# Kernel optimization log

Measured on AMD Instinct MI355X. Metric: run time of the kernel, lower is better.

## Reference

```python
import jax, jax.numpy as jnp
import numpy as np

N = 100000
E = 1600000
IN_C, HID, HEADS, OUT_C = 128, 64, 4, 2
NEG_SLOPE = 0.2


def setup_inputs() -> dict:
    key = jax.random.key(0)
    ks = jax.random.split(key, 10)
    def glorot(k, shape):
        fan = shape[0] + shape[-1]
        return jax.random.uniform(k, shape, jnp.float32, -1.0, 1.0) * np.sqrt(6.0 / fan)
    x = jax.random.normal(ks[0], (N, IN_C), jnp.float32)
    edge_index = jax.random.randint(ks[1], (2, E), 0, N, jnp.int64)
    return {
        "x": x,
        "edge_index": edge_index,
        "W1": glorot(ks[2], (IN_C, HID)),
        "b1": jnp.zeros((HID,), jnp.float32),
        "W2": glorot(ks[3], (HID, HEADS * HID)),
        "att_src": glorot(ks[4], (HEADS, HID)) ,
        "att_dst": glorot(ks[5], (HEADS, HID)),
        "b2": jnp.zeros((HEADS * HID,), jnp.float32),
        "W3": glorot(ks[6], (HEADS * HID, OUT_C)),
        "b3": jnp.zeros((OUT_C,), jnp.float32),
    }


def _add_self_loops(edge_index, n):
    loop = jnp.arange(n, dtype=edge_index.dtype)
    src = jnp.concatenate([edge_index[0], loop])
    dst = jnp.concatenate([edge_index[1], loop])
    return src, dst


def gcn_conv(x, W, b, src, dst, n):
    # x' = X W, then symmetric deg-normalized scatter-add (self-loops included)
    xw = x @ W
    deg = jax.ops.segment_sum(jnp.ones_like(dst, dtype=xw.dtype), dst, num_segments=n)
    dinv = jnp.where(deg > 0, jax.lax.rsqrt(deg), 0.0)
    norm = dinv[src] * dinv[dst]                      # [E2]
    out = jax.ops.segment_sum(xw[src] * norm[:, None], dst, num_segments=n)
    return out + b


def gat_conv(x, W, att_src, att_dst, b, src, dst, n, heads, ch):
    xw = (x @ W).reshape(n, heads, ch)                # [N, H, C]
    a_s = (xw * att_src).sum(-1)                      # [N, H]
    a_d = (xw * att_dst).sum(-1)
    e = jax.nn.leaky_relu(a_s[src] + a_d[dst], NEG_SLOPE)   # [E2, H]
    # segment softmax over incoming edges per destination node
    m = jax.ops.segment_max(e, dst, num_segments=n)
    m = jnp.where(jnp.isfinite(m), m, 0.0)
    e = jnp.exp(e - m[dst])
    den = jax.ops.segment_sum(e, dst, num_segments=n)
    alpha = e / (den[dst] + 1e-16)                    # [E2, H]
    out = jax.ops.segment_sum(xw[src] * alpha[:, :, None], dst, num_segments=n)
    return out.reshape(n, heads * ch) + b


def reference(x, edge_index, W1, b1, W2, att_src, att_dst, b2, W3, b3):
    n = x.shape[0]
    src, dst = _add_self_loops(edge_index, n)
    h = jax.nn.relu(gcn_conv(x, W1, b1, src, dst, n))
    h = jax.nn.elu(gat_conv(h, W2, att_src, att_dst, b2, src, dst, n, HEADS, HID))
    return gcn_conv(h, W3, b3, src, dst, n)
```

## Files before the change

### kernel.cpp

```cpp
#include <hip/hip_runtime.h>
#include <math.h>

#define N_NODES 100000
#define N_EDGES 1600000
#define E2      (N_NODES + N_EDGES)
#define IN_C    128
#define HID     64
#define HEADS   4
#define HH      256
#define OUT_C   2
#define NEG_SLOPE 0.2f

#define SB   1024
#define NSB  ((N_NODES + SB - 1) / SB)
#define NRANGE 8
#define RDIV   12500
#define BINS   RDIV
#define NBK    100
#define CHUNK  (N_EDGES / NBK)
#define CITER  ((CHUNK + 255) / 256)
#define NHB    (NRANGE * NBK)
#define RT     10
#define NT1    6250
#define NGEMM1 ((NT1 + 3) / 4)

typedef __attribute__((ext_vector_type(8))) short bf16x8;
typedef __attribute__((ext_vector_type(4))) float f32x4;

__device__ __forceinline__ float bf2f(unsigned short u) {
    return __uint_as_float(((unsigned)u) << 16);
}
__device__ __forceinline__ unsigned short f2bf(float f) {
    unsigned u = __float_as_uint(f);
    u += 0x7fffu + ((u >> 16) & 1u);
    return (unsigned short)(u >> 16);
}


__global__ __launch_bounds__(256) void k_prep(const float* __restrict__ W2,
        const float* __restrict__ W1,
        const float* __restrict__ att_src, const float* __restrict__ att_dst,
        unsigned short* __restrict__ W2t, unsigned short* __restrict__ wsdt,
        unsigned short* __restrict__ W1t) {
    int b = blockIdx.x, t = threadIdx.x;
    if (b < 64) {
        int g = b * 256 + t;
        int k = g >> 8, n = g & 255;
        W2t[n * 64 + k] = f2bf(W2[g]);
        return;
    }
    if (b < 66) {
        int g = (b - 64) * 256 + t;
        wsdt[512 + g] = 0;
        int k = g >> 3, o = g & 7;
        int h = o & 3;
        const float* att = (o < 4) ? att_src : att_dst;
        float acc = 0.f;
        const float* wrow = W2 + (size_t)k * HH + h * 64;
        const float* arow = att + h * 64;
        for (int c = 0; c < 64; ++c) acc = fmaf(wrow[c], arow[c], acc);
        wsdt[o * 64 + k] = f2bf(acc);
        return;
    }
    int g = (b - 66) * 256 + t;
    int k = g >> 6, n = g & 63;
    W1t[n * 128 + k] = f2bf(W1[g]);
}

__global__ __launch_bounds__(256) void k_hista(const int* __restrict__ ei,
        unsigned short* __restrict__ hp16,
        const float* __restrict__ x, const unsigned short* __restrict__ W1t,
        unsigned short* __restrict__ xw1b) {
    __shared__ unsigned int hh[BINS];
    int b = blockIdx.x, t = threadIdx.x;
    if (b < NHB) {
        int r = b / NBK, k = b - r * NBK;
        for (int i = t; i < BINS; i += 256) hh[i] = 0u;
        __syncthreads();
        const int* dp = ei + N_EDGES + (size_t)k * CHUNK;
        int lo = r * RDIV;
        for (int it = 0; it < CITER; ++it) {
            int idx = it * 256 + t;
            if (idx < CHUNK) {
                int d = dp[idx] - lo;
                if ((unsigned)d < (unsigned)RDIV) atomicAdd(&hh[d], 1u);
            }
        }
        __syncthreads();
        unsigned short* hp = hp16 + (size_t)b * BINS;
        for (int i = t; i < BINS; i += 256) hp[i] = (unsigned short)hh[i];
        return;
    }
    int lane = t & 63, wv = t >> 6;
    int m = lane & 15, quad = lane >> 4;
    bf16x8 B[4][4];
#pragma unroll
    for (int ct = 0; ct < 4; ++ct)
#pragma unroll
        for (int ks = 0; ks < 4; ++ks)
            B[ct][ks] = *(const bf16x8*)(W1t + (size_t)(ct * 16 + m) * IN_C
                                         + ks * 32 + quad * 8);
    int tile = (b - NHB) * 4 + wv;
    if (tile >= NT1) return;
    int rbase = tile * 16;
    const float* xp = x + (size_t)(rbase + m) * IN_C + quad * 8;
    f32x4 c0 = {0.f, 0.f, 0.f, 0.f}, c1 = c0, c2 = c0, c3 = c0;
#pragma unroll
    for (int ks = 0; ks < 4; ++ks) {
        float4 f0 = *(const float4*)(xp + ks * 32);
        float4 f1 = *(const float4*)(xp + ks * 32 + 4);
        bf16x8 a;
        a[0] = (short)f2bf(f0.x); a[1] = (short)f2bf(f0.y);
        a[2] = (short)f2bf(f0.z); a[3] = (short)f2bf(f0.w);
        a[4] = (short)f2bf(f1.x); a[5] = (short)f2bf(f1.y);
        a[6] = (short)f2bf(f1.z); a[7] = (short)f2bf(f1.w);
        c0 = __builtin_amdgcn_mfma_f32_16x16x32_bf16(a, B[0][ks], c0, 0, 0, 0);
        c1 = __builtin_amdgcn_mfma_f32_16x16x32_bf16(a, B[1][ks], c1, 0, 0, 0);
        c2 = __builtin_amdgcn_mfma_f32_16x16x32_bf16(a, B[2][ks], c2, 0, 0, 0);
        c3 = __builtin_amdgcn_mfma_f32_16x16x32_bf16(a, B[3][ks], c3, 0, 0, 0);
    }
    int row0 = rbase + quad * 4;
#pragma unroll
    for (int ct = 0; ct < 4; ++ct) {
        f32x4 c = (ct == 0) ? c0 : (ct == 1) ? c1 : (ct == 2) ? c2 : c3;
        unsigned short* p = xw1b + (size_t)row0 * HID + ct * 16 + m;
#pragma unroll
        for (int r = 0; r < 4; ++r) p[(size_t)r * HID] = f2bf(c[r]);
    }
}

__global__ __launch_bounds__(256) void k_scan1(unsigned short* __restrict__ hp16,
        int* __restrict__ cnt, int* __restrict__ bsum) {
    int b = blockIdx.x, t = threadIdx.x;
    int s = 0;
#pragma unroll
    for (int u = 0; u < 4; ++u) {
        int i = b * SB + u * 256 + t;
        if (i < N_NODES) {
            int r = i / RDIV, bin = i - r * RDIV;
            unsigned short* p = hp16 + (size_t)r * NBK * BINS + bin;
            unsigned acc = 0;
            for (int k = 0; k < NBK; ++k) {
                unsigned short hv = p[(size_t)k * BINS];
                p[(size_t)k * BINS] = (unsigned short)acc;
                acc += hv;
            }
            cnt[i] = (int)acc;
            s += (int)acc + 1;
        }
    }
#pragma unroll
    for (int off = 1; off < 64; off <<= 1) s += __shfl_xor(s, off);
    __shared__ int wsum[4];
    int lane = t & 63, wv = t >> 6;
    if (lane == 0) wsum[wv] = s;
    __syncthreads();
    if (t == 0) bsum[b] = (wsum[0] + wsum[1]) + (wsum[2] + wsum[3]);
}

__global__ __launch_bounds__(256) void k_scan3(const int* __restrict__ cnt,
        const int* __restrict__ bsum, int* __restrict__ rowptr,
        float* __restrict__ dinv, int* __restrict__ col) {
    int b = blockIdx.x, t = threadIdx.x;
    int lane = t & 63, wv = t >> 6;
    __shared__ int wred[4];
    {
        int v = (t < b) ? bsum[t] : 0;
#pragma unroll
        for (int off = 1; off < 64; off <<= 1) v += __shfl_xor(v, off);
        if (lane == 0) wred[wv] = v;
    }
    __syncthreads();
    int pre = (wred[0] + wred[1]) + (wred[2] + wred[3]);
    __syncthreads();

    int i = b * SB + t * 4;
    int c0 = 0, c1 = 0, c2 = 0, c3 = 0;
    if (i + 3 < N_NODES) {
        int4 v = *(const int4*)(cnt + i);
        c0 = v.x; c1 = v.y; c2 = v.z; c3 = v.w;
    } else if (i < N_NODES) {
        c0 = cnt[i];
        if (i + 1 < N_NODES) c1 = cnt[i + 1];
        if (i + 2 < N_NODES) c2 = cnt[i + 2];
    }
    int n0 = (i < N_NODES), n1 = (i + 1 < N_NODES),
        n2 = (i + 2 < N_NODES), n3 = (i + 3 < N_NODES);
    int d0 = c0 + n0, d1 = c1 + n1, d2 = c2 + n2, d3 = c3 + n3;
    int s = (d0 + d1) + (d2 + d3);
    int inc = s;
#pragma unroll
    for (int off = 1; off < 64; off <<= 1) {
        int u = __shfl_up(inc, off);
        if (lane >= off) inc += u;
    }
    __shared__ int wtot[4];
    if (lane == 63) wtot[wv] = inc;
    __syncthreads();
    int base = pre + (inc - s);
    for (int w = 0; w < wv; ++w) base += wtot[w];
    if (n0) { rowptr[i]     = base;                dinv[i]     = rsqrtf((float)d0); col[base] = i; }
    if (n1) { rowptr[i + 1] = base + d0;           dinv[i + 1] = rsqrtf((float)d1); col[base + d0] = i + 1; }
    if (n2) { rowptr[i + 2] = base + d0 + d1;      dinv[i + 2] = rsqrtf((float)d2); col[base + d0 + d1] = i + 2; }
    if (n3) { rowptr[i + 3] = base + d0 + d1 + d2; dinv[i + 3] = rsqrtf((float)d3); col[base + d0 + d1 + d2] = i + 3; }
    if (b == 0 && t == 0) rowptr[N_NODES] = E2;
}

__global__ __launch_bounds__(256) void k_fillb(const int* __restrict__ ei,
        const int* __restrict__ rowptr, const unsigned short* __restrict__ hp16,
        int* __restrict__ col) {
    __shared__ unsigned int cur[BINS];
    int b = blockIdx.x, t = threadIdx.x;
    int r = b / NBK, k = b - r * NBK;
    int lo = r * RDIV;
    const unsigned short* pp = hp16 + (size_t)b * BINS;
    for (int i = t; i < BINS; i += 256)
        cur[i] = (unsigned)rowptr[lo + i] + 1u + (unsigned)pp[i];
    __syncthreads();
    const int* dp = ei + N_EDGES + (size_t)k * CHUNK;
    const int* sp = ei + (size_t)k * CHUNK;
    for (int it = 0; it < CITER; ++it) {
        int idx = it * 256 + t;
        if (idx < CHUNK) {
            int d = dp[idx] - lo;
            if ((unsigned)d < (unsigned)RDIV) {
                unsigned pos = atomicAdd(&cur[d], 1u);
                col[pos] = sp[idx];
            }
        }
    }
}

__global__ __launch_bounds__(256) void k_agg1(const int* __restrict__ rowptr,
        const int* __restrict__ col, const unsigned short* __restrict__ xw1b,
        const float* __restrict__ dinv, const float* __restrict__ b1,
        unsigned short* __restrict__ h1b) {
    int t = threadIdx.x;
    int lane = t & 63;
    int d = blockIdx.x * 4 + (t >> 6);
    if (d >= N_NODES) return;
    int start = rowptr[d], end = rowptr[d + 1];
    int sub = lane >> 4;
    int cpos = lane & 15;
    float4 acc = make_float4(0.f, 0.f, 0.f, 0.f);
    for (int base = start; base < end; base += 64) {
        int cnt = min(64, end - base);
        int sl = (base + lane < end) ? col[base + lane] : 0;
#pragma unroll 2
        for (int j = 0; j < cnt; j += 4) {
            int idx = j + sub;
            int sj = __shfl(sl, idx);
            if (idx < cnt) {
                float di = dinv[sj];
                ushort4 v = ((const ushort4*)(xw1b + (size_t)sj * HID))[cpos];
                acc.x = fmaf(di, bf2f(v.x), acc.x);
                acc.y = fmaf(di, bf2f(v.y), acc.y);
                acc.z = fmaf(di, bf2f(v.z), acc.z);
                acc.w = fmaf(di, bf2f(v.w), acc.w);
            }
        }
    }
    acc.x += __shfl_xor(acc.x, 16); acc.y += __shfl_xor(acc.y, 16);
    acc.z += __shfl_xor(acc.z, 16); acc.w += __shfl_xor(acc.w, 16);
    acc.x += __shfl_xor(acc.x, 32); acc.y += __shfl_xor(acc.y, 32);
    acc.z += __shfl_xor(acc.z, 32); acc.w += __shfl_xor(acc.w, 32);
    if (lane < 16) {
        float di = dinv[d];
        float4 b = ((const float4*)b1)[lane];
        float ox = fmaf(acc.x, di, b.x); ox = ox > 0.f ? ox : 0.f;
        float oy = fmaf(acc.y, di, b.y); oy = oy > 0.f ? oy : 0.f;
        float oz = fmaf(acc.z, di, b.z); oz = oz > 0.f ? oz : 0.f;
        float ow = fmaf(acc.w, di, b.w); ow = ow > 0.f ? ow : 0.f;
        ushort4 o = make_ushort4(f2bf(ox), f2bf(oy), f2bf(oz), f2bf(ow));
        ((ushort4*)(h1b + (size_t)d * HID))[lane] = o;
    }
}

__global__ __launch_bounds__(256) void k_attn(const unsigned short* __restrict__ h1b,
        const unsigned short* __restrict__ wsdt,
        float* __restrict__ a_s, float* __restrict__ a_d) {
    int t = threadIdx.x;
    int lane = t & 63, wv = t >> 6;
    int m = lane & 15, quad = lane >> 4;
    bf16x8 Bw0 = *(const bf16x8*)(wsdt + (size_t)m * 64 + quad * 8);
    bf16x8 Bw1 = *(const bf16x8*)(wsdt + (size_t)m * 64 + 32 + quad * 8);
    int tile = blockIdx.x * 4 + wv;
    if (tile >= NT1) return;
    int rbase = tile * 16;
    const unsigned short* ap = h1b + (size_t)(rbase + m) * 64 + quad * 8;
    bf16x8 a0 = *(const bf16x8*)(ap);
    bf16x8 a1 = *(const bf16x8*)(ap + 32);
    f32x4 aw = {0.f, 0.f, 0.f, 0.f};
    aw = __builtin_amdgcn_mfma_f32_16x16x32_bf16(a0, Bw0, aw, 0, 0, 0);
    aw = __builtin_amdgcn_mfma_f32_16x16x32_bf16(a1, Bw1, aw, 0, 0, 0);
    int row = rbase + quad * 4;
    if (m < 4) {
#pragma unroll
        for (int r = 0; r < 4; ++r) a_s[(row + r) * 4 + m] = aw[r];
    } else if (m < 8) {
#pragma unroll
        for (int r = 0; r < 4; ++r) a_d[(row + r) * 4 + (m - 4)] = aw[r];
    }
}

__global__ __launch_bounds__(256) void k_agg2u(const int* __restrict__ rowptr,
        const int* __restrict__ col, const unsigned short* __restrict__ h1b,
        const float* __restrict__ a_s, const float* __restrict__ a_d,
        unsigned short* __restrict__ ub, int dbase) {
    __shared__ int   ss[4][64];
    __shared__ float sp[4][64][4];
    int t = threadIdx.x;
    int lane = t & 63, wv = t >> 6;
    int d = dbase + blockIdx.x * 4 + wv;
    if (d >= N_NODES) return;
    const float4* as4 = (const float4*)a_s;
    float4 adv = ((const float4*)a_d)[d];
    int start = rowptr[d], end = rowptr[d + 1];

    float den0 = 0.f, den1 = 0.f, den2 = 0.f, den3 = 0.f;
    float acc0 = 0.f, acc1 = 0.f, acc2 = 0.f, acc3 = 0.f;
    for (int base = start; base < end; base += 64) {
        int cnt = min(64, end - base);
        float p0 = 0.f, p1 = 0.f, p2 = 0.f, p3 = 0.f;
        int s = 0;
        if (lane < cnt) {
            s = col[base + lane];
            float4 av = as4[s];
            float v;
            v = av.x + adv.x; v = v > 0.f ? v : NEG_SLOPE * v; p0 = __expf(v);
            v = av.y + adv.y; v = v > 0.f ? v : NEG_SLOPE * v; p1 = __expf(v);
            v = av.z + adv.z; v = v > 0.f ? v : NEG_SLOPE * v; p2 = __expf(v);
            v = av.w + adv.w; v = v > 0.f ? v : NEG_SLOPE * v; p3 = __expf(v);
            den0 += p0; den1 += p1; den2 += p2; den3 += p3;
        }
        ss[wv][lane] = s;
        ((float4*)sp[wv])[lane] = make_float4(p0, p1, p2, p3);
#pragma unroll 4
        for (int j = 0; j < cnt; ++j) {
            int sj = ss[wv][j];
            float4 pj = ((const float4*)sp[wv])[j];
            float v = bf2f(h1b[(unsigned)sj * 64u + (unsigned)lane]);
            acc0 = fmaf(pj.x, v, acc0);
            acc1 = fmaf(pj.y, v, acc1);
            acc2 = fmaf(pj.z, v, acc2);
            acc3 = fmaf(pj.w, v, acc3);
        }
    }
#pragma unroll
    for (int mk = 1; mk < 64; mk <<= 1) {
        den0 += __shfl_xor(den0, mk);
        den1 += __shfl_xor(den1, mk);
        den2 += __shfl_xor(den2, mk);
        den3 += __shfl_xor(den3, mk);
    }
    float u0 = acc0 / (den0 + 1e-16f);
    float u1 = acc1 / (den1 + 1e-16f);
    float u2 = acc2 / (den2 + 1e-16f);
    float u3 = acc3 / (den3 + 1e-16f);
    unsigned short* up = ub + (size_t)d * HH;
    up[lane]       = f2bf(u0);
    up[64 + lane]  = f2bf(u1);
    up[128 + lane] = f2bf(u2);
    up[192 + lane] = f2bf(u3);
}

__global__ __launch_bounds__(256) void k_gemm3m(const unsigned short* __restrict__ ub,
        const unsigned short* __restrict__ W2t, const float* __restrict__ b2,
        const float* __restrict__ W3, const float* __restrict__ dinv,
        float2* __restrict__ xw3) {
    int t = threadIdx.x;
    int lane = t & 63, wv = t >> 6;
    int m = lane & 15, quad = lane >> 4;
    int nb = wv * 64 + m;
    bf16x8 B[4][2];
#pragma unroll
    for (int ct = 0; ct < 4; ++ct)
#pragma unroll
        for (int ks = 0; ks < 2; ++ks)
            B[ct][ks] = *(const bf16x8*)(W2t + (size_t)(nb + ct * 16) * 64
                                         + ks * 32 + quad * 8);
    float bv[4]; float2 w3v[4];
#pragma unroll
    for (int ct = 0; ct < 4; ++ct) {
        int n = nb + ct * 16;
        bv[ct] = b2[n];
        w3v[ct] = ((const float2*)W3)[n];
    }
    __shared__ float red[4][16][2];
    int r0 = blockIdx.x * (RT * 16);
    for (int tile = 0; tile < RT; ++tile) {
        int rbase = r0 + tile * 16;
        const unsigned short* ap = ub + (size_t)(rbase + m) * HH + wv * 64 + quad * 8;
        bf16x8 a0 = *(const bf16x8*)(ap);
        bf16x8 a1 = *(const bf16x8*)(ap + 32);
        f32x4 c0 = {0.f, 0.f, 0.f, 0.f}, c1 = c0, c2 = c0, c3 = c0;
        c0 = __builtin_amdgcn_mfma_f32_16x16x32_bf16(a0, B[0][0], c0, 0, 0, 0);
        c1 = __builtin_amdgcn_mfma_f32_16x16x32_bf16(a0, B[1][0], c1, 0, 0, 0);
        c2 = __builtin_amdgcn_mfma_f32_16x16x32_bf16(a0, B[2][0], c2, 0, 0, 0);
        c3 = __builtin_amdgcn_mfma_f32_16x16x32_bf16(a0, B[3][0], c3, 0, 0, 0);
        c0 = __builtin_amdgcn_mfma_f32_16x16x32_bf16(a1, B[0][1], c0, 0, 0, 0);
        c1 = __builtin_amdgcn_mfma_f32_16x16x32_bf16(a1, B[1][1], c1, 0, 0, 0);
        c2 = __builtin_amdgcn_mfma_f32_16x16x32_bf16(a1, B[2][1], c2, 0, 0, 0);
        c3 = __builtin_amdgcn_mfma_f32_16x16x32_bf16(a1, B[3][1], c3, 0, 0, 0);
        float px[4] = {0.f, 0.f, 0.f, 0.f}, py[4] = {0.f, 0.f, 0.f, 0.f};
#pragma unroll
        for (int ct = 0; ct < 4; ++ct) {
            f32x4 c = (ct == 0) ? c0 : (ct == 1) ? c1 : (ct == 2) ? c2 : c3;
#pragma unroll
            for (int r = 0; r < 4; ++r) {
                float o = c[r] + bv[ct];
                o = o > 0.f ? o : expm1f(o);
                px[r] = fmaf(o, w3v[ct].x, px[r]);
                py[r] = fmaf(o, w3v[ct].y, py[r]);
            }
        }
#pragma unroll
        for (int mk = 1; mk < 16; mk <<= 1) {
#pragma unroll
            for (int r = 0; r < 4; ++r) {
                px[r] += __shfl_xor(px[r], mk);
                py[r] += __shfl_xor(py[r], mk);
            }
        }
        if (m == 0) {
#pragma unroll
            for (int r = 0; r < 4; ++r) {
                red[wv][quad * 4 + r][0] = px[r];
                red[wv][quad * 4 + r][1] = py[r];
            }
        }
        __syncthreads();
        if (t < 32) {
            int row = t >> 1, xy = t & 1;
            float s = red[0][row][xy] + red[1][row][xy]
                    + red[2][row][xy] + red[3][row][xy];
            ((float*)(xw3 + (rbase + row)))[xy] = s * dinv[rbase + row];
        }
        __syncthreads();
    }
}

__global__ __launch_bounds__(256) void k_agg3(const int* __restrict__ rowptr,
        const int* __restrict__ col, const float2* __restrict__ xw3,
        const float* __restrict__ dinv, const float* __restrict__ b3,
        float* __restrict__ out) {
    int t = threadIdx.x;
    int lane = t & 63;
    int g = lane >> 2, s = lane & 3;
    int d = blockIdx.x * 64 + (t >> 6) * 16 + g;
    if (d >= N_NODES) return;
    int e0 = rowptr[d], e1 = rowptr[d + 1];
    float a0 = 0.f, a1 = 0.f;
    for (int e = e0 + s; e < e1; e += 4) {
        float2 v = xw3[col[e]];
        a0 += v.x; a1 += v.y;
    }
    a0 += __shfl_xor(a0, 1); a1 += __shfl_xor(a1, 1);
    a0 += __shfl_xor(a0, 2); a1 += __shfl_xor(a1, 2);
    if (s == 0) {
        float di = dinv[d];
        out[d * 2 + 0] = fmaf(a0, di, b3[0]);
        out[d * 2 + 1] = fmaf(a1, di, b3[1]);
    }
}


extern "C" void kernel_launch(void* const* d_in, const int* in_sizes, int n_in,
                              void* d_out, int out_size, void* d_ws, size_t ws_size,
                              hipStream_t stream) {
    const float* x       = (const float*)d_in[0];
    const int*   ei      = (const int*)d_in[1];
    const float* W1      = (const float*)d_in[2];
    const float* b1      = (const float*)d_in[3];
    const float* W2      = (const float*)d_in[4];
    const float* att_src = (const float*)d_in[5];
    const float* att_dst = (const float*)d_in[6];
    const float* b2      = (const float*)d_in[7];
    const float* W3      = (const float*)d_in[8];
    const float* b3      = (const float*)d_in[9];
    float* out = (float*)d_out;
    (void)in_sizes; (void)n_in; (void)out_size; (void)ws_size;

    char* ws = (char*)d_ws;
    size_t off = 0;
    auto alloc = [&](size_t bytes) -> void* {
        void* p = ws + off;
        off = (off + bytes + 255) & ~(size_t)255;
        return p;
    };
    int*    rowptr = (int*)alloc((N_NODES + 1) * sizeof(int));
    int*    cnt    = (int*)alloc(N_NODES * sizeof(int));
    int*    bsum   = (int*)alloc(NSB * sizeof(int));
    int*    col    = (int*)alloc((size_t)E2 * sizeof(int));
    float*  dinv   = (float*)alloc(N_NODES * sizeof(float));
    unsigned short* W2t  = (unsigned short*)alloc(64 * 256 * sizeof(unsigned short));
    unsigned short* wsdt = (unsigned short*)alloc(16 * 64 * sizeof(unsigned short));
    unsigned short* W1t  = (unsigned short*)alloc(64 * 128 * sizeof(unsigned short));
    unsigned short* xw1b = (unsigned short*)alloc((size_t)N_NODES * HID * sizeof(unsigned short));
    unsigned short* h1b  = (unsigned short*)alloc((size_t)N_NODES * HID * sizeof(unsigned short));
    float*  a_s    = (float*)alloc((size_t)N_NODES * HEADS * sizeof(float));
    float*  a_d    = (float*)alloc((size_t)N_NODES * HEADS * sizeof(float));
    unsigned short* ub   = (unsigned short*)alloc((size_t)N_NODES * HH * sizeof(unsigned short));
    float2* xw3    = (float2*)alloc((size_t)N_NODES * sizeof(float2));
    unsigned short* hp16 = ub;

    k_prep<<<98, 256, 0, stream>>>(W2, W1, att_src, att_dst, W2t, wsdt, W1t);
    k_hista<<<NHB + NGEMM1, 256, 0, stream>>>(ei, hp16, x, W1t, xw1b);
    k_scan1<<<NSB, 256, 0, stream>>>(hp16, cnt, bsum);
    k_scan3<<<NSB, 256, 0, stream>>>(cnt, bsum, rowptr, dinv, col);
    k_fillb<<<NHB, 256, 0, stream>>>(ei, rowptr, hp16, col);

    k_agg1<<<(N_NODES + 3) / 4, 256, 0, stream>>>(rowptr, col, xw1b, dinv, b1, h1b);
    k_attn<<<(NT1 + 3) / 4, 256, 0, stream>>>(h1b, wsdt, a_s, a_d);
    const int HALF = 50000;
    k_agg2u<<<HALF / 4, 256, 0, stream>>>(rowptr, col, h1b, a_s, a_d, ub, 0);
    k_agg2u<<<(N_NODES - HALF + 3) / 4, 256, 0, stream>>>(rowptr, col, h1b, a_s, a_d, ub, HALF);
    k_gemm3m<<<(N_NODES / 16) / RT, 256, 0, stream>>>(ub, W2t, b2, W3, dinv, xw3);
    k_agg3<<<(N_NODES + 63) / 64, 256, 0, stream>>>(rowptr, col, xw3, dinv, b3, out);
}
```

Baseline: 426.5 us.

## Record per-edge histogram ranks to make CSR fill atomic-free

The histogram pass now saves each edge's local atomic rank within its chunk and destination bin into a 16-bit array. The fill kernel then computes each edge's column slot directly from rowptr, the per-chunk prefix and the saved rank, with no shared-memory atomics. This removes the contended LDS atomics and the per-block 12500-entry cursor initialisation from the fill step. In exchange the histogram pass writes an extra array, and the new fill launches 8x6250 blocks where most threads exit early because their destination is outside the block's range. The fill also makes more scattered global reads of hp16.

```diff
diff --git a/kernel.cpp b/kernel.cpp
--- a/kernel.cpp
+++ b/kernel.cpp
@@ -20,6 +20,7 @@
 #define CHUNK  (N_EDGES / NBK)
 #define CITER  ((CHUNK + 255) / 256)
 #define NHB    (NRANGE * NBK)
+#define NFC    (N_EDGES / 256)
 #define RT     10
 #define NT1    6250
 #define NGEMM1 ((NT1 + 3) / 4)
@@ -68,7 +69,7 @@
 }
 
 __global__ __launch_bounds__(256) void k_hista(const int* __restrict__ ei,
-        unsigned short* __restrict__ hp16,
+        unsigned short* __restrict__ hp16, unsigned short* __restrict__ rank16,
         const float* __restrict__ x, const unsigned short* __restrict__ W1t,
         unsigned short* __restrict__ xw1b) {
     __shared__ unsigned int hh[BINS];
@@ -78,12 +79,16 @@
         for (int i = t; i < BINS; i += 256) hh[i] = 0u;
         __syncthreads();
         const int* dp = ei + N_EDGES + (size_t)k * CHUNK;
+        unsigned short* rp = rank16 + (size_t)k * CHUNK;
         int lo = r * RDIV;
         for (int it = 0; it < CITER; ++it) {
             int idx = it * 256 + t;
             if (idx < CHUNK) {
                 int d = dp[idx] - lo;
-                if ((unsigned)d < (unsigned)RDIV) atomicAdd(&hh[d], 1u);
+                if ((unsigned)d < (unsigned)RDIV) {
+                    unsigned rk = atomicAdd(&hh[d], 1u);
+                    rp[idx] = (unsigned short)rk;
+                }
             }
         }
         __syncthreads();
@@ -206,29 +211,21 @@
     if (b == 0 && t == 0) rowptr[N_NODES] = E2;
 }
 
-__global__ __launch_bounds__(256) void k_fillb(const int* __restrict__ ei,
-        const int* __restrict__ rowptr, const unsigned short* __restrict__ hp16,
-        int* __restrict__ col) {
-    __shared__ unsigned int cur[BINS];
-    int b = blockIdx.x, t = threadIdx.x;
-    int r = b / NBK, k = b - r * NBK;
-    int lo = r * RDIV;
-    const unsigned short* pp = hp16 + (size_t)b * BINS;
-    for (int i = t; i < BINS; i += 256)
-        cur[i] = (unsigned)rowptr[lo + i] + 1u + (unsigned)pp[i];
-    __syncthreads();
-    const int* dp = ei + N_EDGES + (size_t)k * CHUNK;
-    const int* sp = ei + (size_t)k * CHUNK;
-    for (int it = 0; it < CITER; ++it) {
-        int idx = it * 256 + t;
-        if (idx < CHUNK) {
-            int d = dp[idx] - lo;
-            if ((unsigned)d < (unsigned)RDIV) {
-                unsigned pos = atomicAdd(&cur[d], 1u);
-                col[pos] = sp[idx];
-            }
-        }
-    }
+__global__ void k_fill(const int* __restrict__ ei, const int* __restrict__ rowptr,
+        const unsigned short* __restrict__ hp16,
+        const unsigned short* __restrict__ rank16, int* __restrict__ col) {
+    int b = blockIdx.x;
+    int r = b / NFC;
+    int c = b - r * NFC;
+    int i = c * 256 + threadIdx.x;
+    int d = ei[N_EDGES + i];
+    int bin = d - r * RDIV;
+    if ((unsigned)bin >= (unsigned)RDIV) return;
+    int k = i / CHUNK;
+    unsigned pos = (unsigned)rowptr[d] + 1u
+                 + (unsigned)hp16[(size_t)(r * NBK + k) * BINS + bin]
+                 + (unsigned)rank16[i];
+    col[pos] = ei[i];
 }
 
 __global__ __launch_bounds__(256) void k_agg1(const int* __restrict__ rowptr,
@@ -502,13 +499,14 @@
     float*  a_d    = (float*)alloc((size_t)N_NODES * HEADS * sizeof(float));
     unsigned short* ub   = (unsigned short*)alloc((size_t)N_NODES * HH * sizeof(unsigned short));
     float2* xw3    = (float2*)alloc((size_t)N_NODES * sizeof(float2));
-    unsigned short* hp16 = ub;
+    unsigned short* hp16   = ub;
+    unsigned short* rank16 = ub + (size_t)NHB * BINS;
 
     k_prep<<<98, 256, 0, stream>>>(W2, W1, att_src, att_dst, W2t, wsdt, W1t);
-    k_hista<<<NHB + NGEMM1, 256, 0, stream>>>(ei, hp16, x, W1t, xw1b);
+    k_hista<<<NHB + NGEMM1, 256, 0, stream>>>(ei, hp16, rank16, x, W1t, xw1b);
     k_scan1<<<NSB, 256, 0, stream>>>(hp16, cnt, bsum);
     k_scan3<<<NSB, 256, 0, stream>>>(cnt, bsum, rowptr, dinv, col);
-    k_fillb<<<NHB, 256, 0, stream>>>(ei, rowptr, hp16, col);
+    k_fill<<<NRANGE * NFC, 256, 0, stream>>>(ei, rowptr, hp16, rank16, col);
 
     k_agg1<<<(N_NODES + 3) / 4, 256, 0, stream>>>(rowptr, col, xw1b, dinv, b1, h1b);
     k_attn<<<(NT1 + 3) / 4, 256, 0, stream>>>(h1b, wsdt, a_s, a_d);
```

New measurement: 400.9 us. -6.0%, faster.
